# Kernel tuning notes

Measured on AMD Instinct MI355X. Metric: run time of the kernel, lower is better.

The kernel has to match this reference:

```python
import jax, jax.numpy as jnp
import numpy as np

N, E, EMB, HID, H = 50000, 800000, 128, 512, 8
D = EMB // H
EPS = 1e-5


def _linear_params(key, fan_in, fan_out):
    s = 1.0 / np.sqrt(fan_in)
    k1, k2 = jax.random.split(key)
    w = jax.random.uniform(k1, (fan_in, fan_out), minval=-s, maxval=s, dtype=jnp.float32)
    b = jax.random.uniform(k2, (fan_out,), minval=-s, maxval=s, dtype=jnp.float32)
    return w, b


def setup_inputs() -> dict:
    key = jax.random.key(0)
    ks = jax.random.split(key, 9)
    x = jax.random.normal(ks[0], (N, EMB), dtype=jnp.float32)
    edge_index = jax.random.randint(ks[1], (2, E), 0, N, dtype=jnp.int32)
    batch = jnp.zeros((N,), dtype=jnp.int32)
    wq, bq = _linear_params(ks[2], EMB, EMB)
    wk, bk = _linear_params(ks[3], EMB, EMB)
    wv, bv = _linear_params(ks[4], EMB, EMB)
    wo, bo = _linear_params(ks[5], EMB, EMB)
    w1, b1 = _linear_params(ks[6], EMB, HID)
    w2, b2 = _linear_params(ks[7], HID, EMB)
    g1 = jnp.ones((EMB,), jnp.float32); be1 = jnp.zeros((EMB,), jnp.float32)
    g2 = jnp.ones((EMB,), jnp.float32); be2 = jnp.zeros((EMB,), jnp.float32)
    return {"x": x, "wq": wq, "bq": bq, "wk": wk, "bk": bk, "wv": wv, "bv": bv,
            "wo": wo, "bo": bo, "w1": w1, "b1": b1, "w2": w2, "b2": b2,
            "g1": g1, "be1": be1, "g2": g2, "be2": be2,
            "edge_index": edge_index, "batch": batch, "latent": 0}


def _batchnorm(x, g, b):
    mu = x.mean(axis=0)
    var = ((x - mu) ** 2).mean(axis=0)  # biased, as BatchNorm1d in training
    return g * (x - mu) * jax.lax.rsqrt(var + EPS) + b


def _forward(x, wq, bq, wk, bk, wv, bv, wo, bo, w1, b1, w2, b2, g1, be1, g2, be2, A, B):
    n = x.shape[0]
    q = (x @ wq + bq).reshape(n, H, D)
    k = (x @ wk + bk).reshape(n, H, D)
    v = (x @ wv + bv).reshape(n, H, D)
    # per-edge head-mixing scores: q[A] @ k[B]^T -> [E, H, H]
    score = jnp.einsum('ehd,egd->ehg', q[A], k[B])
    ssum = jax.ops.segment_sum(score, A, num_segments=n)
    cnt = jax.ops.segment_sum(jnp.ones((A.shape[0],), score.dtype), A, num_segments=n)
    score = ssum / jnp.maximum(cnt, 1.0)[:, None, None]  # scatter-mean per node [N,H,H]
    score = jax.nn.softmax(score, axis=-1)
    out = jnp.einsum('ehg,egd->ehd', score, v).reshape(n, EMB)
    out = out @ wo + bo
    x = _batchnorm(out + x, g1, be1)
    h = jax.nn.gelu(x @ w1 + b1, approximate=False)
    h = h @ w2 + b2
    x = _batchnorm(h + x, g2, be2)
    return x


def reference(x, wq, bq, wk, bk, wv, bv, wo, bo, w1, b1, w2, b2, g1, be1, g2, be2, edge_index, batch, latent):
    A, B = edge_index[0], edge_index[1]
    return _forward(x, wq, bq, wk, bk, wv, bv, wo, bo, w1, b1, w2, b2, g1, be1, g2, be2, A, B)
```

## Files before the change

kernel.cpp:

```cpp
#include <hip/hip_runtime.h>
#include <hip/hip_bf16.h>

typedef float f4 __attribute__((ext_vector_type(4)));
typedef short bh8 __attribute__((ext_vector_type(8)));

#define EMB 128
#define HID 512

__device__ __forceinline__ float bfbits2f(unsigned int lo16) {
    unsigned int u = lo16 << 16;
    return __builtin_bit_cast(float, u);
}
__device__ __forceinline__ short f2bf(float f) {
    __hip_bfloat16 h = __float2bfloat16(f);
    return __builtin_bit_cast(short, h);
}

__global__ void hist_kernel(const int* __restrict__ edge, unsigned* __restrict__ cnt, int E) {
    int stride = gridDim.x * blockDim.x;
    for (int e = blockIdx.x * blockDim.x + threadIdx.x; e < E; e += stride)
        atomicAdd(&cnt[edge[e]], 1u);
}

__global__ void scan_blocks(const unsigned* __restrict__ cnt, int* __restrict__ off,
                            int* __restrict__ bsum, int n) {
    __shared__ int ls[256];
    int tid = threadIdx.x;
    int base = blockIdx.x * 1024 + tid * 4;
    int v0 = 0, v1 = 0, v2 = 0, v3 = 0;
    if (base + 0 < n) v0 = (int)cnt[base + 0];
    if (base + 1 < n) v1 = (int)cnt[base + 1];
    if (base + 2 < n) v2 = (int)cnt[base + 2];
    if (base + 3 < n) v3 = (int)cnt[base + 3];
    int s = v0 + v1 + v2 + v3;
    ls[tid] = s;
    __syncthreads();
    for (int d = 1; d < 256; d <<= 1) {
        int t = (tid >= d) ? ls[tid - d] : 0;
        __syncthreads();
        ls[tid] += t;
        __syncthreads();
    }
    int incl = ls[tid];
    int run = incl - s;
    if (tid == 255) bsum[blockIdx.x] = incl;
    if (base + 0 < n) { off[base + 0] = run; run += v0; }
    if (base + 1 < n) { off[base + 1] = run; run += v1; }
    if (base + 2 < n) { off[base + 2] = run; run += v2; }
    if (base + 3 < n) { off[base + 3] = run; }
}

__global__ void scan_bsums(int* __restrict__ bsum, int nb) {
    int lane = threadIdx.x & 63;
    int x = (lane < nb) ? bsum[lane] : 0;
    int orig = x;
#pragma unroll
    for (int o = 1; o < 64; o <<= 1) {
        int t = __shfl_up(x, o, 64);
        if (lane >= o) x += t;
    }
    if (lane < nb) bsum[lane] = x - orig;
}

__global__ void scan_apply(const unsigned* __restrict__ cnt, const int* __restrict__ bsum,
                           int* __restrict__ off, int* __restrict__ offw,
                           float* __restrict__ cntf, int n) {
    int base = blockIdx.x * 1024 + threadIdx.x * 4;
    int add = bsum[blockIdx.x];
#pragma unroll
    for (int i = 0; i < 4; ++i) {
        int idx = base + i;
        if (idx < n) {
            int o = off[idx] + add;
            off[idx] = o;
            offw[idx] = o;
            cntf[idx] = (float)cnt[idx];
        }
    }
}

__global__ void place_kernel(const int* __restrict__ edge, int* __restrict__ offw,
                             int* __restrict__ sortedB, int E) {
    int stride = gridDim.x * blockDim.x;
    for (int e = blockIdx.x * blockDim.x + threadIdx.x; e < E; e += stride) {
        int a = edge[e];
        int pos = atomicAdd(&offw[a], 1);
        sortedB[pos] = edge[E + e];
    }
}

__global__ void prep_all(const float* __restrict__ wq, const float* __restrict__ wk,
                         const float* __restrict__ wv, const float* __restrict__ wo,
                         const float* __restrict__ w1, const float* __restrict__ w2,
                         const float* __restrict__ bq, const float* __restrict__ bk,
                         const float* __restrict__ bv,
                         short* __restrict__ wqkvT, short* __restrict__ woT,
                         short* __restrict__ w1T, short* __restrict__ w2T,
                         float* __restrict__ bqkv) {
    int id = blockIdx.x * blockDim.x + threadIdx.x;
    if (id < 16384) {
        int k = id >> 7, c = id & 127;
        wqkvT[c * 128 + k] = f2bf(wq[id]);
    } else if (id < 32768) {
        int t = id - 16384; int k = t >> 7, c = t & 127;
        wqkvT[(128 + c) * 128 + k] = f2bf(wk[t]);
    } else if (id < 49152) {
        int t = id - 32768; int k = t >> 7, c = t & 127;
        wqkvT[(256 + c) * 128 + k] = f2bf(wv[t]);
    } else if (id < 65536) {
        int t = id - 49152; int k = t >> 7, c = t & 127;
        woT[c * 128 + k] = f2bf(wo[t]);
    } else if (id < 131072) {
        int t = id - 65536; int k = t >> 9, c = t & 511;
        w1T[c * 128 + k] = f2bf(w1[t]);
    } else if (id < 196608) {
        int t = id - 131072; int k = t >> 7, c = t & 127;
        w2T[c * 512 + k] = f2bf(w2[t]);
    }
    if (id < 128) {
        bqkv[id] = bq[id];
        bqkv[128 + id] = bk[id];
        bqkv[256 + id] = bv[id];
    }
}

template<int KT, bool IN_BF16>
__device__ __forceinline__ void ld_ab(bh8 (&av)[4], bh8 (&bv)[4],
                                      const float* __restrict__ Xf, const short* __restrict__ Xb,
                                      const int (&rowA)[4], const short* __restrict__ Wt,
                                      int C0, int l15, int kbase) {
#pragma unroll
    for (int rf = 0; rf < 4; ++rf) {
        if constexpr (IN_BF16) {
            av[rf] = *(const bh8*)(Xb + (size_t)rowA[rf] * KT + kbase);
        } else {
            f4 lo = *(const f4*)(Xf + (size_t)rowA[rf] * KT + kbase);
            f4 hi = *(const f4*)(Xf + (size_t)rowA[rf] * KT + kbase + 4);
            bh8 t;
            t[0] = f2bf(lo[0]); t[1] = f2bf(lo[1]); t[2] = f2bf(lo[2]); t[3] = f2bf(lo[3]);
            t[4] = f2bf(hi[0]); t[5] = f2bf(hi[1]); t[6] = f2bf(hi[2]); t[7] = f2bf(hi[3]);
            av[rf] = t;
        }
    }
#pragma unroll
    for (int cf = 0; cf < 4; ++cf)
        bv[cf] = *(const bh8*)(Wt + (size_t)(C0 + cf * 16 + l15) * KT + kbase);
}

__device__ __forceinline__ void mm16(f4 (&acc)[4][4], const bh8 (&av)[4], const bh8 (&bv)[4]) {
#pragma unroll
    for (int rf = 0; rf < 4; ++rf)
#pragma unroll
        for (int cf = 0; cf < 4; ++cf)
            acc[rf][cf] = __builtin_amdgcn_mfma_f32_16x16x32_bf16(av[rf], bv[cf], acc[rf][cf], 0, 0, 0);
}

#define CSTRIDE 136

template<int KT, bool IN_BF16, bool GELU, bool OUT_BF16, bool RESID, bool RBF16, bool STATS>
__global__ __launch_bounds__(256, 2) void mfma_gemm(
    const void* __restrict__ Xv, const short* __restrict__ Wt, const float* __restrict__ bias,
    const void* __restrict__ resid,
    void* __restrict__ outv, float* __restrict__ slots, int n, int OC, int ncolb, int nrb)
{
    int bx, by;
    if (ncolb == 1) {
        bx = blockIdx.x; by = 0;
    } else {
        int q = blockIdx.x >> 3;
        by = q % ncolb;
        bx = (q / ncolb) * 8 + (blockIdx.x & 7);
        if (bx >= nrb) return;
    }
    const int lane = threadIdx.x & 63;
    const int w = threadIdx.x >> 6;
    const int wr = w >> 1, wc = w & 1;
    const int R0 = bx * 128 + wr * 64;
    const int C0 = by * 128 + wc * 64;
    const int l15 = lane & 15;
    const int kg = lane >> 4;

    const float* Xf = (const float*)Xv;
    const short* Xb = (const short*)Xv;

    int rowA[4];
#pragma unroll
    for (int rf = 0; rf < 4; ++rf) rowA[rf] = min(R0 + rf * 16 + l15, n - 1);

    f4 acc[4][4];
#pragma unroll
    for (int rf = 0; rf < 4; ++rf)
#pragma unroll
        for (int cf = 0; cf < 4; ++cf) acc[rf][cf] = 0.f;

    constexpr int NT = KT / 32;
    bh8 aA[4], bA[4], aB[4], bB[4];

    ld_ab<KT, IN_BF16>(aA, bA, Xf, Xb, rowA, Wt, C0, l15, kg * 8);
#pragma unroll
    for (int t = 0; t < NT; t += 2) {
        ld_ab<KT, IN_BF16>(aB, bB, Xf, Xb, rowA, Wt, C0, l15, (t + 1) * 32 + kg * 8);
        mm16(acc, aA, bA);
        if (t + 2 < NT)
            ld_ab<KT, IN_BF16>(aA, bA, Xf, Xb, rowA, Wt, C0, l15, (t + 2) * 32 + kg * 8);
        mm16(acc, aB, bB);
    }

    if constexpr (OUT_BF16) {
        extern __shared__ short cs[];
        const int lrb = wr * 64;
        const int lcb = wc * 64;
#pragma unroll
        for (int cf = 0; cf < 4; ++cf) {
            const float bcol = bias[C0 + cf * 16 + l15];
#pragma unroll
            for (int rf = 0; rf < 4; ++rf) {
#pragma unroll
                for (int i = 0; i < 4; ++i) {
                    float val = acc[rf][cf][i] + bcol;
                    if constexpr (GELU) val = 0.5f * val * (1.0f + erff(val * 0.70710678f));
                    cs[(lrb + rf * 16 + kg * 4 + i) * CSTRIDE + lcb + cf * 16 + l15] = f2bf(val);
                }
            }
        }
        __syncthreads();
        const int tc = threadIdx.x & 15;
        const int tr = threadIdx.x >> 4;
        const int gcb = by * 128;
#pragma unroll
        for (int r = 0; r < 8; ++r) {
            int lrow = tr + r * 16;
            int grow = bx * 128 + lrow;
            if (grow < n) {
                bh8 v = *(bh8*)(cs + lrow * CSTRIDE + tc * 8);
                *(bh8*)((short*)outv + (size_t)grow * OC + gcb + tc * 8) = v;
            }
        }
    } else {
#pragma unroll
        for (int cf = 0; cf < 4; ++cf) {
            const int col = C0 + cf * 16 + l15;
            const float bcol = bias[col];
#pragma unroll
            for (int rf = 0; rf < 4; ++rf) {
                float s = 0.f, q = 0.f;
#pragma unroll
                for (int i = 0; i < 4; ++i) {
                    const int row = R0 + rf * 16 + kg * 4 + i;
                    if (row < n) {
                        float val = acc[rf][cf][i] + bcol;
                        if constexpr (RESID) {
                            float rv;
                            if constexpr (RBF16)
                                rv = bfbits2f((unsigned short)((const short*)resid)[(size_t)row * EMB + col]);
                            else
                                rv = ((const float*)resid)[(size_t)row * EMB + col];
                            val += rv;
                        }
                        if constexpr (GELU) val = 0.5f * val * (1.0f + erff(val * 0.70710678f));
                        if constexpr (STATS) { s += val; q += val * val; }
                        ((float*)outv)[(size_t)row * OC + col] = val;
                    }
                }
                if constexpr (STATS) {
                    s += __shfl_xor(s, 16, 64); s += __shfl_xor(s, 32, 64);
                    q += __shfl_xor(q, 16, 64); q += __shfl_xor(q, 32, 64);
                    if (kg == 0) {
                        float* sl = slots + (size_t)(bx & 63) * 256;
                        unsafeAtomicAdd(&sl[col], s);
                        unsafeAtomicAdd(&sl[128 + col], q);
                    }
                }
            }
        }
    }
}

__global__ __launch_bounds__(256, 2) void ffn_fused(
    const short* __restrict__ xn1, const short* __restrict__ w1T, const float* __restrict__ b1,
    const short* __restrict__ w2T, const float* __restrict__ b2,
    float* __restrict__ y2, float* __restrict__ slots, int n)
{
    extern __shared__ short hs[];
    const int bx = blockIdx.x;
    const int lane = threadIdx.x & 63;
    const int w = threadIdx.x >> 6;
    const int wr = w >> 1, wc = w & 1;
    const int R0 = bx * 128 + wr * 64;
    const int l15 = lane & 15;
    const int kg = lane >> 4;

    int rowA[4];
#pragma unroll
    for (int rf = 0; rf < 4; ++rf) rowA[rf] = min(R0 + rf * 16 + l15, n - 1);

    f4 acc2[4][4];
#pragma unroll
    for (int rf = 0; rf < 4; ++rf)
#pragma unroll
        for (int cf = 0; cf < 4; ++cf) acc2[rf][cf] = 0.f;

    for (int c = 0; c < 4; ++c) {
        f4 acc1[4][4];
#pragma unroll
        for (int rf = 0; rf < 4; ++rf)
#pragma unroll
            for (int cf = 0; cf < 4; ++cf) acc1[rf][cf] = 0.f;
#pragma unroll
        for (int ks = 0; ks < 4; ++ks) {
            const int kbase = ks * 32 + kg * 8;
            bh8 a1[4], b1f[4];
#pragma unroll
            for (int rf = 0; rf < 4; ++rf)
                a1[rf] = *(const bh8*)(xn1 + (size_t)rowA[rf] * EMB + kbase);
#pragma unroll
            for (int cf = 0; cf < 4; ++cf) {
                int col = c * 128 + wc * 64 + cf * 16 + l15;
                b1f[cf] = *(const bh8*)(w1T + (size_t)col * EMB + kbase);
            }
            mm16(acc1, a1, b1f);
        }
        __syncthreads();
        {
            const int lrb = wr * 64;
            const int lcb = wc * 64;
#pragma unroll
            for (int cf = 0; cf < 4; ++cf) {
                const float bcol = b1[c * 128 + wc * 64 + cf * 16 + l15];
#pragma unroll
                for (int rf = 0; rf < 4; ++rf) {
#pragma unroll
                    for (int i = 0; i < 4; ++i) {
                        float val = acc1[rf][cf][i] + bcol;
                        val = 0.5f * val * (1.0f + erff(val * 0.70710678f));
                        hs[(lrb + rf * 16 + kg * 4 + i) * CSTRIDE + lcb + cf * 16 + l15] = f2bf(val);
                    }
                }
            }
        }
        __syncthreads();
#pragma unroll
        for (int ks = 0; ks < 4; ++ks) {
            const int kbase = ks * 32 + kg * 8;
            bh8 a2[4], b2f[4];
#pragma unroll
            for (int rf = 0; rf < 4; ++rf)
                a2[rf] = *(const bh8*)(hs + (wr * 64 + rf * 16 + l15) * CSTRIDE + kbase);
#pragma unroll
            for (int cf = 0; cf < 4; ++cf) {
                int col = wc * 64 + cf * 16 + l15;
                b2f[cf] = *(const bh8*)(w2T + (size_t)col * HID + c * 128 + kbase);
            }
            mm16(acc2, a2, b2f);
        }
    }

    const int C0 = wc * 64;
#pragma unroll
    for (int cf = 0; cf < 4; ++cf) {
        const int col = C0 + cf * 16 + l15;
        const float bcol = b2[col];
#pragma unroll
        for (int rf = 0; rf < 4; ++rf) {
            float s = 0.f, q = 0.f;
#pragma unroll
            for (int i = 0; i < 4; ++i) {
                const int row = R0 + rf * 16 + kg * 4 + i;
                if (row < n) {
                    float val = acc2[rf][cf][i] + bcol;
                    val += bfbits2f((unsigned short)xn1[(size_t)row * EMB + col]);
                    s += val; q += val * val;
                    y2[(size_t)row * EMB + col] = val;
                }
            }
            s += __shfl_xor(s, 16, 64); s += __shfl_xor(s, 32, 64);
            q += __shfl_xor(q, 16, 64); q += __shfl_xor(q, 32, 64);
            if (kg == 0) {
                float* sl = slots + (size_t)(bx & 63) * 256;
                unsafeAtomicAdd(&sl[col], s);
                unsafeAtomicAdd(&sl[128 + col], q);
            }
        }
    }
}

__global__ void gather_attn_kernel(const short* __restrict__ qkv, const int* __restrict__ off,
                                   const unsigned* __restrict__ cnt, const int* __restrict__ sortedB,
                                   const float* __restrict__ cntf, short* __restrict__ attno, int n) {
    int wid = (int)((blockIdx.x * blockDim.x + threadIdx.x) >> 6);
    int lane = threadIdx.x & 63;
    int nw = (gridDim.x * blockDim.x) >> 6;
    const int l15 = lane & 15;
    const int grp = lane >> 4;
    const int h = lane >> 3, g = lane & 7;
    for (int node = wid; node < n; node += nw) {
        int start = off[node];
        int deg = (int)cnt[node];
        float a[8];
#pragma unroll
        for (int i = 0; i < 8; ++i) a[i] = 0.f;
        for (int j = 0; j < deg; j += 8) {
            int i0 = j + grp, i1 = j + 4 + grp;
            uint4 u0 = make_uint4(0, 0, 0, 0), u1 = make_uint4(0, 0, 0, 0);
            if (i0 < deg) {
                int b = sortedB[start + i0];
                u0 = *(const uint4*)(qkv + (size_t)b * 384 + 128 + l15 * 8);
            }
            if (i1 < deg) {
                int b = sortedB[start + i1];
                u1 = *(const uint4*)(qkv + (size_t)b * 384 + 128 + l15 * 8);
            }
            unsigned w0[4] = {u0.x, u0.y, u0.z, u0.w};
            unsigned w1[4] = {u1.x, u1.y, u1.z, u1.w};
#pragma unroll
            for (int i = 0; i < 4; ++i) {
                a[2 * i]     += bfbits2f(w0[i] & 0xffffu) + bfbits2f(w1[i] & 0xffffu);
                a[2 * i + 1] += bfbits2f(w0[i] >> 16)     + bfbits2f(w1[i] >> 16);
            }
        }
#pragma unroll
        for (int i = 0; i < 8; ++i) {
            a[i] += __shfl_xor(a[i], 16, 64);
            a[i] += __shfl_xor(a[i], 32, 64);
        }

        const short* qp = qkv + (size_t)node * 384 + h * 16;
        uint4 qa = *(const uint4*)qp;
        uint4 qb = *(const uint4*)(qp + 8);
        float qv[16];
        {
            unsigned ua[4] = {qa.x, qa.y, qa.z, qa.w};
            unsigned ub[4] = {qb.x, qb.y, qb.z, qb.w};
#pragma unroll
            for (int w2 = 0; w2 < 4; ++w2) {
                qv[2 * w2]         = bfbits2f(ua[w2] & 0xffffu);
                qv[2 * w2 + 1]     = bfbits2f(ua[w2] >> 16);
                qv[8 + 2 * w2]     = bfbits2f(ub[w2] & 0xffffu);
                qv[8 + 2 * w2 + 1] = bfbits2f(ub[w2] >> 16);
            }
        }
        float s = 0.f;
#pragma unroll
        for (int i = 0; i < 8; ++i) {
            s += qv[i]     * __shfl(a[i], 2 * g, 64);
            s += qv[8 + i] * __shfl(a[i], 2 * g + 1, 64);
        }
        float c = cntf[node];
        s *= 1.0f / fmaxf(c, 1.0f);
        float m = s;
#pragma unroll
        for (int o = 1; o < 8; o <<= 1) m = fmaxf(m, __shfl_xor(m, o, 64));
        float e = __expf(s - m);
        float sum = e;
#pragma unroll
        for (int o = 1; o < 8; o <<= 1) sum += __shfl_xor(sum, o, 64);
        float p = e / sum;
        float o0 = 0.f, o1 = 0.f;
        int d0 = g * 2;
#pragma unroll
        for (int gg = 0; gg < 8; ++gg) {
            float pg = __shfl(p, h * 8 + gg, 64);
            unsigned vv = *(const unsigned*)(qkv + (size_t)node * 384 + 256 + gg * 16 + d0);
            o0 += pg * bfbits2f(vv & 0xffffu);
            o1 += pg * bfbits2f(vv >> 16);
        }
        unsigned pk = (unsigned)(unsigned short)f2bf(o0) | ((unsigned)(unsigned short)f2bf(o1) << 16);
        *(unsigned*)(attno + (size_t)node * EMB + h * 16 + d0) = pk;
    }
}

__global__ void bn_finalize_slots(const float* __restrict__ slots, float* __restrict__ scsh,
                                  const float* __restrict__ g, const float* __restrict__ be, int n) {
    int c = threadIdx.x;
    float s = 0.f, q = 0.f;
    for (int i = 0; i < 64; ++i) {
        s += slots[(size_t)i * 256 + c];
        q += slots[(size_t)i * 256 + 128 + c];
    }
    float invn = 1.0f / (float)n;
    float mean = s * invn;
    float var = fmaxf(q * invn - mean * mean, 0.f);
    float sc = g[c] * rsqrtf(var + 1e-5f);
    scsh[c] = sc;
    scsh[128 + c] = be[c] - mean * sc;
}

__global__ void apply_bn_bf16(const float* __restrict__ Y, const float* __restrict__ scsh,
                              short* __restrict__ out, size_t total8) {
    size_t stride = (size_t)gridDim.x * blockDim.x;
    for (size_t i = (size_t)blockIdx.x * blockDim.x + threadIdx.x; i < total8; i += stride) {
        size_t base = i * 8;
        f4 lo = *(const f4*)(Y + base);
        f4 hi = *(const f4*)(Y + base + 4);
        int c = (int)(base & 127);
        f4 s0 = *(const f4*)(scsh + c);
        f4 s1 = *(const f4*)(scsh + c + 4);
        f4 h0 = *(const f4*)(scsh + 128 + c);
        f4 h1 = *(const f4*)(scsh + 128 + c + 4);
        lo = lo * s0 + h0;
        hi = hi * s1 + h1;
        bh8 o;
        o[0] = f2bf(lo[0]); o[1] = f2bf(lo[1]); o[2] = f2bf(lo[2]); o[3] = f2bf(lo[3]);
        o[4] = f2bf(hi[0]); o[5] = f2bf(hi[1]); o[6] = f2bf(hi[2]); o[7] = f2bf(hi[3]);
        *(bh8*)(out + base) = o;
    }
}

__global__ void bn_apply(float* __restrict__ Y, const float* __restrict__ scsh, size_t total4) {
    size_t stride = (size_t)gridDim.x * blockDim.x;
    for (size_t i = (size_t)blockIdx.x * blockDim.x + threadIdx.x; i < total4; i += stride) {
        f4 vv = ((f4*)Y)[i];
        int c = (int)((i * 4) & 127);
#pragma unroll
        for (int j = 0; j < 4; ++j) vv[j] = vv[j] * scsh[c + j] + scsh[128 + c + j];
        ((f4*)Y)[i] = vv;
    }
}

extern "C" void kernel_launch(void* const* d_in, const int* in_sizes, int n_in,
                              void* d_out, int out_size, void* d_ws, size_t ws_size,
                              hipStream_t stream) {
    const float* x   = (const float*)d_in[0];
    const float* wq  = (const float*)d_in[1];
    const float* bq  = (const float*)d_in[2];
    const float* wk  = (const float*)d_in[3];
    const float* bk  = (const float*)d_in[4];
    const float* wv  = (const float*)d_in[5];
    const float* bv  = (const float*)d_in[6];
    const float* wo  = (const float*)d_in[7];
    const float* bo  = (const float*)d_in[8];
    const float* w1  = (const float*)d_in[9];
    const float* b1  = (const float*)d_in[10];
    const float* w2  = (const float*)d_in[11];
    const float* b2  = (const float*)d_in[12];
    const float* g1  = (const float*)d_in[13];
    const float* be1 = (const float*)d_in[14];
    const float* g2  = (const float*)d_in[15];
    const float* be2 = (const float*)d_in[16];
    const int* edge  = (const int*)d_in[17];

    int n = in_sizes[0] / EMB;
    int E = in_sizes[17] / 2;

    float* wsf = (float*)d_ws;
    unsigned* cnt_u = (unsigned*)wsf;
    float*  cntf  = wsf + 65536;
    int*    off   = (int*)(wsf + 2 * 65536);
    int*    offw  = (int*)(wsf + 3 * 65536);
    int*    bsum  = (int*)(wsf + 4 * 65536);
    int*    sortedB = (int*)(wsf + 4 * 65536 + 64);
    float*  base5 = wsf + 4 * 65536 + 64 + E;
    short*  qkv   = (short*)base5;
    short*  attno = (short*)(base5 + (size_t)n * 256);
    float*  y1    = base5 + (size_t)n * 320;
    float*  warea = y1 + (size_t)n * 128;
    short*  wqkvT = (short*)warea;
    short*  woT   = wqkvT + 384 * 128;
    short*  w1T   = woT + 128 * 128;
    short*  w2T   = w1T + 512 * 128;
    float*  bqkv  = (float*)(w2T + 128 * 512);
    float*  slots1 = bqkv + 384;
    float*  slots2 = slots1 + 64 * 256;
    float*  scsh1  = slots2 + 64 * 256;
    float*  scsh2  = scsh1 + 256;
    short*  xn1   = attno;
    float*  y2    = (float*)d_out;

    hipMemsetAsync(cnt_u, 0, 65536 * sizeof(unsigned), stream);
    hipMemsetAsync(slots1, 0, 2 * 64 * 256 * sizeof(float), stream);

    int nb = (n + 1023) / 1024;
    hist_kernel<<<2048, 256, 0, stream>>>(edge, cnt_u, E);
    scan_blocks<<<nb, 256, 0, stream>>>(cnt_u, off, bsum, n);
    scan_bsums<<<1, 64, 0, stream>>>(bsum, nb);
    scan_apply<<<nb, 256, 0, stream>>>(cnt_u, bsum, off, offw, cntf, n);
    place_kernel<<<2048, 256, 0, stream>>>(edge, offw, sortedB, E);

    prep_all<<<768, 256, 0, stream>>>(wq, wk, wv, wo, w1, w2, bq, bk, bv,
                                      wqkvT, woT, w1T, w2T, bqkv);

    int nrb = (n + 127) / 128;
    int nrb8 = ((nrb + 7) / 8) * 8;
    const size_t CSH = 128 * CSTRIDE * sizeof(short);

    mfma_gemm<128, false, false, true, false, false, false><<<nrb8 * 3, 256, CSH, stream>>>(
        x, wqkvT, bqkv, nullptr, qkv, nullptr, n, 384, 3, nrb);

    gather_attn_kernel<<<2048, 256, 0, stream>>>(qkv, off, cnt_u, sortedB, cntf, attno, n);

    mfma_gemm<128, true, false, false, true, false, true><<<nrb, 256, 0, stream>>>(
        attno, woT, bo, x, y1, slots1, n, EMB, 1, nrb);

    bn_finalize_slots<<<1, 128, 0, stream>>>(slots1, scsh1, g1, be1, n);

    apply_bn_bf16<<<1600, 256, 0, stream>>>(y1, scsh1, xn1, (size_t)n * EMB / 8);

    ffn_fused<<<nrb, 256, CSH, stream>>>(xn1, w1T, b1, w2T, b2, y2, slots2, n);

    bn_finalize_slots<<<1, 128, 0, stream>>>(slots2, scsh2, g2, be2, n);
    bn_apply<<<512, 256, 0, stream>>>(y2, scsh2, (size_t)n * EMB / 4);
}
```

Measured before the change: 308.8 us.

## Retile fused FFN to per-warp 32-row strips and use tanh-form GELU

The fused FFN kernel is restructured so each wave owns 32 full rows and all 128 columns. Its input A fragments now stay in registers across all hidden chunks, and each wave keeps a private LDS slice for the hidden activations, which removes both block-level __syncthreads barriers. Exact erf GELU is replaced everywhere by a sigmoid/tanh approximation built on __expf, which cuts transcendental cost but changes numerics relative to the exact-GELU reference. Each wave now loads every W tile for its own rows, so weight fragment traffic per wave goes up.

After: 325.0 us. 1.05x slower.

```diff
diff --git a/kernel.cpp b/kernel.cpp
--- a/kernel.cpp
+++ b/kernel.cpp
@@ -14,6 +14,11 @@
 __device__ __forceinline__ short f2bf(float f) {
     __hip_bfloat16 h = __float2bfloat16(f);
     return __builtin_bit_cast(short, h);
+}
+__device__ __forceinline__ float gelu_fast(float x) {
+    float x3 = x * x * x;
+    float y = 1.5957691216f * x + 0.0713548163f * x3;
+    return x / (1.0f + __expf(-y));
 }
 
 __global__ void hist_kernel(const int* __restrict__ edge, unsigned* __restrict__ cnt, int E) {
@@ -218,7 +223,7 @@
 #pragma unroll
                 for (int i = 0; i < 4; ++i) {
                     float val = acc[rf][cf][i] + bcol;
-                    if constexpr (GELU) val = 0.5f * val * (1.0f + erff(val * 0.70710678f));
+                    if constexpr (GELU) val = gelu_fast(val);
                     cs[(lrb + rf * 16 + kg * 4 + i) * CSTRIDE + lcb + cf * 16 + l15] = f2bf(val);
                 }
             }
@@ -257,7 +262,7 @@
                                 rv = ((const float*)resid)[(size_t)row * EMB + col];
                             val += rv;
                         }
-                        if constexpr (GELU) val = 0.5f * val * (1.0f + erff(val * 0.70710678f));
+                        if constexpr (GELU) val = gelu_fast(val);
                         if constexpr (STATS) { s += val; q += val * val; }
                         ((float*)outv)[(size_t)row * OC + col] = val;
                     }
@@ -285,83 +290,91 @@
     const int bx = blockIdx.x;
     const int lane = threadIdx.x & 63;
     const int w = threadIdx.x >> 6;
-    const int wr = w >> 1, wc = w & 1;
-    const int R0 = bx * 128 + wr * 64;
+    const int R0 = bx * 128 + w * 32;
     const int l15 = lane & 15;
     const int kg = lane >> 4;
-
-    int rowA[4];
-#pragma unroll
-    for (int rf = 0; rf < 4; ++rf) rowA[rf] = min(R0 + rf * 16 + l15, n - 1);
-
-    f4 acc2[4][4];
-#pragma unroll
-    for (int rf = 0; rf < 4; ++rf)
-#pragma unroll
-        for (int cf = 0; cf < 4; ++cf) acc2[rf][cf] = 0.f;
+    short* myh = hs + w * 32 * CSTRIDE;
+
+    int rowA[2];
+#pragma unroll
+    for (int rf = 0; rf < 2; ++rf) rowA[rf] = min(R0 + rf * 16 + l15, n - 1);
+
+    bh8 aF[4][2];
+#pragma unroll
+    for (int rf = 0; rf < 2; ++rf) {
+        const short* p = xn1 + (size_t)rowA[rf] * EMB + kg * 8;
+        aF[0][rf] = *(const bh8*)(p);
+        aF[1][rf] = *(const bh8*)(p + 32);
+        aF[2][rf] = *(const bh8*)(p + 64);
+        aF[3][rf] = *(const bh8*)(p + 96);
+    }
+
+    f4 acc2[2][8];
+#pragma unroll
+    for (int rf = 0; rf < 2; ++rf)
+#pragma unroll
+        for (int cf = 0; cf < 8; ++cf) acc2[rf][cf] = 0.f;
 
     for (int c = 0; c < 4; ++c) {
-        f4 acc1[4][4];
-#pragma unroll
-        for (int rf = 0; rf < 4; ++rf)
-#pragma unroll
-            for (int cf = 0; cf < 4; ++cf) acc1[rf][cf] = 0.f;
+        f4 acc1[2][8];
+#pragma unroll
+        for (int rf = 0; rf < 2; ++rf)
+#pragma unroll
+            for (int cf = 0; cf < 8; ++cf) acc1[rf][cf] = 0.f;
+
 #pragma unroll
         for (int ks = 0; ks < 4; ++ks) {
-            const int kbase = ks * 32 + kg * 8;
-            bh8 a1[4], b1f[4];
-#pragma unroll
-            for (int rf = 0; rf < 4; ++rf)
-                a1[rf] = *(const bh8*)(xn1 + (size_t)rowA[rf] * EMB + kbase);
-#pragma unroll
-            for (int cf = 0; cf < 4; ++cf) {
-                int col = c * 128 + wc * 64 + cf * 16 + l15;
-                b1f[cf] = *(const bh8*)(w1T + (size_t)col * EMB + kbase);
-            }
-            mm16(acc1, a1, b1f);
-        }
-        __syncthreads();
-        {
-            const int lrb = wr * 64;
-            const int lcb = wc * 64;
-#pragma unroll
-            for (int cf = 0; cf < 4; ++cf) {
-                const float bcol = b1[c * 128 + wc * 64 + cf * 16 + l15];
-#pragma unroll
-                for (int rf = 0; rf < 4; ++rf) {
-#pragma unroll
-                    for (int i = 0; i < 4; ++i) {
-                        float val = acc1[rf][cf][i] + bcol;
-                        val = 0.5f * val * (1.0f + erff(val * 0.70710678f));
-                        hs[(lrb + rf * 16 + kg * 4 + i) * CSTRIDE + lcb + cf * 16 + l15] = f2bf(val);
-                    }
+            bh8 bF[8];
+#pragma unroll
+            for (int cf = 0; cf < 8; ++cf) {
+                int col = c * 128 + cf * 16 + l15;
+                bF[cf] = *(const bh8*)(w1T + (size_t)col * EMB + ks * 32 + kg * 8);
+            }
+#pragma unroll
+            for (int rf = 0; rf < 2; ++rf)
+#pragma unroll
+                for (int cf = 0; cf < 8; ++cf)
+                    acc1[rf][cf] = __builtin_amdgcn_mfma_f32_16x16x32_bf16(aF[ks][rf], bF[cf], acc1[rf][cf], 0, 0, 0);
+        }
+
+#pragma unroll
+        for (int cf = 0; cf < 8; ++cf) {
+            const float bcol = b1[c * 128 + cf * 16 + l15];
+#pragma unroll
+            for (int rf = 0; rf < 2; ++rf) {
+#pragma unroll
+                for (int i = 0; i < 4; ++i) {
+                    float val = gelu_fast(acc1[rf][cf][i] + bcol);
+                    myh[(rf * 16 + kg * 4 + i) * CSTRIDE + cf * 16 + l15] = f2bf(val);
                 }
             }
         }
-        __syncthreads();
+
 #pragma unroll
         for (int ks = 0; ks < 4; ++ks) {
-            const int kbase = ks * 32 + kg * 8;
-            bh8 a2[4], b2f[4];
-#pragma unroll
-            for (int rf = 0; rf < 4; ++rf)
-                a2[rf] = *(const bh8*)(hs + (wr * 64 + rf * 16 + l15) * CSTRIDE + kbase);
-#pragma unroll
-            for (int cf = 0; cf < 4; ++cf) {
-                int col = wc * 64 + cf * 16 + l15;
-                b2f[cf] = *(const bh8*)(w2T + (size_t)col * HID + c * 128 + kbase);
-            }
-            mm16(acc2, a2, b2f);
-        }
-    }
-
-    const int C0 = wc * 64;
-#pragma unroll
-    for (int cf = 0; cf < 4; ++cf) {
-        const int col = C0 + cf * 16 + l15;
+            bh8 aH[2], bF[8];
+#pragma unroll
+            for (int rf = 0; rf < 2; ++rf)
+                aH[rf] = *(const bh8*)(myh + (rf * 16 + l15) * CSTRIDE + ks * 32 + kg * 8);
+#pragma unroll
+            for (int cf = 0; cf < 8; ++cf) {
+                int col = cf * 16 + l15;
+                bF[cf] = *(const bh8*)(w2T + (size_t)col * HID + c * 128 + ks * 32 + kg * 8);
+            }
+#pragma unroll
+            for (int rf = 0; rf < 2; ++rf)
+#pragma unroll
+                for (int cf = 0; cf < 8; ++cf)
+                    acc2[rf][cf] = __builtin_amdgcn_mfma_f32_16x16x32_bf16(aH[rf], bF[cf], acc2[rf][cf], 0, 0, 0);
+        }
+    }
+
+#pragma unroll
+    for (int cf = 0; cf < 8; ++cf) {
+        const int col = cf * 16 + l15;
         const float bcol = b2[col];
 #pragma unroll
-        for (int rf = 0; rf < 4; ++rf) {
+        for (int rf = 0; rf < 2; ++rf) {
             float s = 0.f, q = 0.f;
 #pragma unroll
             for (int i = 0; i < 4; ++i) {
```
